# Kernel tuning notes

Hardware: AMD Instinct MI355X
Metric: run time of the kernel (lower is better)

Reference implementation:

```python
import jax, jax.numpy as jnp
import numpy as np

B, S, T, D_IN, D_T = 32, 4096, 8192, 128, 256


def _length_mask(key, batch, maxlen, minlen):
    lens = jax.random.randint(key, (batch,), minlen, maxlen + 1)
    lens = lens.at[0].set(maxlen)  # ensure max(t_lens)==maxlen (static t_len)
    return (jnp.arange(maxlen)[None, :] < lens[:, None]).astype(jnp.float32)


def setup_inputs() -> dict:
    key = jax.random.key(0)
    ks = jax.random.split(key, 8)
    student_emb = jax.random.normal(ks[0], (B, S, D_IN), dtype=jnp.float32)
    s_mask = _length_mask(ks[1], B, S, S // 2)
    t_mask = _length_mask(ks[2], B, T, T // 2)
    # params (stored as [in, out] so y = x @ W + b)
    pe_w1 = jax.random.normal(ks[3], (1, 64), dtype=jnp.float32) * 0.1
    pe_b1 = jnp.zeros((64,), dtype=jnp.float32)
    pe_w2 = jax.random.normal(ks[4], (64, D_IN), dtype=jnp.float32) * 0.1
    pe_b2 = jnp.zeros((D_IN,), dtype=jnp.float32)
    pt_w = jax.random.normal(ks[5], (2 * D_IN, D_T), dtype=jnp.float32) * 0.05
    pt_b = jnp.zeros((D_T,), dtype=jnp.float32)
    ln_g = jnp.ones((D_T,), dtype=jnp.float32)
    ln_b = jnp.zeros((D_T,), dtype=jnp.float32)
    neighbor_weights = jnp.ones((3,), dtype=jnp.float32)
    return {
        "student_emb": student_emb, "s_mask": s_mask, "t_mask": t_mask,
        "target_length": T,
        "pe_w1": pe_w1, "pe_b1": pe_b1, "pe_w2": pe_w2, "pe_b2": pe_b2,
        "pt_w": pt_w, "pt_b": pt_b, "ln_g": ln_g, "ln_b": ln_b,
        "neighbor_weights": neighbor_weights,
    }


def _layernorm(x, g, b, eps=1e-5):
    mu = jnp.mean(x, axis=-1, keepdims=True)
    var = jnp.mean(jnp.square(x - mu), axis=-1, keepdims=True)
    return (x - mu) * jax.lax.rsqrt(var + eps) * g + b


def reference(student_emb, s_mask, t_mask, target_length,
              pe_w1, pe_b1, pe_w2, pe_b2, pt_w, pt_b, ln_g, ln_b,
              neighbor_weights):
    batch, s_len, _ = student_emb.shape
    t_len = t_mask.shape[1]  # == max(t_mask.sum(1)) by construction
    s_lens = s_mask.sum(axis=1)  # [B] float
    pos = jnp.linspace(0.0, 1.0, t_len)  # [T]
    pos_grid = jnp.broadcast_to(pos[None, :], (batch, t_len))
    s_pos = pos_grid * (s_lens[:, None] - 1.0)
    curr = s_pos.astype(jnp.int32)                      # floor (nonneg)
    prev = jnp.clip(curr - 1, 0, s_len - 1)
    nxt = jnp.clip(curr + 1, 0, s_len - 1)

    def gat(idx):  # masked gather: [B,T,D]
        e = jnp.take_along_axis(student_emb, idx[..., None], axis=1)
        m = jnp.take_along_axis(s_mask, idx, axis=1)[..., None]
        return e * m

    w = jax.nn.softmax(neighbor_weights)
    blended = w[0] * gat(prev) + w[1] * gat(curr) + w[2] * gat(nxt)

    # position encoder MLP on scalar positions
    h = jax.nn.gelu(pos_grid[..., None] * pe_w1[0] + pe_b1, approximate=False)
    pos_emb = h @ pe_w2 + pe_b2  # [B,T,D_in]

    combined = jnp.concatenate([blended, pos_emb], axis=-1)  # [B,T,2*D_in]
    trans = jax.nn.gelu(combined @ pt_w + pt_b, approximate=False)
    trans = _layernorm(trans, ln_g, ln_b)
    trans = trans * t_mask[:, :t_len, None]
    if t_len < target_length:
        trans = jnp.pad(trans, ((0, 0), (0, target_length - t_len), (0, 0)))
    return trans
```

## Files before the change

### kernel.cpp

```cpp
#include <hip/hip_runtime.h>
#include <math.h>

#define S_LEN 4096
#define T_LEN 8192
#define D_TT  256
#define TILE_M 64
#define NKT   6
#define LDA   264

typedef unsigned short u16;
typedef __attribute__((ext_vector_type(8))) unsigned short u16x8;
typedef __attribute__((ext_vector_type(4))) float f32x4;
typedef __bf16 bf16x8 __attribute__((ext_vector_type(8)));

__device__ __forceinline__ float bf2f(u16 v) {
    union { unsigned u; float f; } x; x.u = ((unsigned)v) << 16; return x.f;
}
__device__ __forceinline__ u16 f2bf(float f) {
    union { float f; unsigned u; } x; x.f = f;
    return (u16)((x.u + 0x7fffu + ((x.u >> 16) & 1u)) >> 16);
}
__device__ __forceinline__ float gelu_f(float x) {
    return 0.5f * x * (1.0f + erff(x * 0.70710678118654752440f));
}

__device__ __forceinline__ bool detect_f32(const void* t_mask) {
    return *(const unsigned*)t_mask == 0x3F800000u;
}

template<bool F32>
__device__ __forceinline__ float ld1(const void* p, size_t i) {
    if constexpr (F32) return ((const float*)p)[i];
    else return bf2f(((const u16*)p)[i]);
}
template<bool F32>
__device__ __forceinline__ void load8(const void* p, size_t idx, float o[8]) {
    if constexpr (F32) {
        const float4* q = (const float4*)((const float*)p + idx);
        float4 a = q[0], b = q[1];
        o[0]=a.x; o[1]=a.y; o[2]=a.z; o[3]=a.w;
        o[4]=b.x; o[5]=b.y; o[6]=b.z; o[7]=b.w;
    } else {
        u16x8 v = *(const u16x8*)((const u16*)p + idx);
        #pragma unroll
        for (int j = 0; j < 8; ++j) o[j] = bf2f(v[j]);
    }
}
template<bool F32>
__device__ __forceinline__ void store8(void* p, size_t idx, const float o[8]) {
    if constexpr (F32) {
        float4 a = {o[0],o[1],o[2],o[3]};
        float4 b = {o[4],o[5],o[6],o[7]};
        float4* q = (float4*)((float*)p + idx);
        q[0] = a; q[1] = b;
    } else {
        u16x8 v;
        #pragma unroll
        for (int j = 0; j < 8; ++j) v[j] = f2bf(o[j]);
        *(u16x8*)((u16*)p + idx) = v;
    }
}


template<bool F32>
__global__ __launch_bounds__(256) void prep_kernel(
    const void* __restrict__ s_mask, const void* __restrict__ t_mask_det,
    const void* __restrict__ nw,
    const void* __restrict__ pe_w2, const void* __restrict__ pe_b2,
    const void* __restrict__ pt_w, const void* __restrict__ pt_b,
    int* __restrict__ ws_len, float* __restrict__ ws_w,
    float* __restrict__ ws_bias, u16* __restrict__ ws_bfrag)
{
    if (detect_f32(t_mask_det) != F32) return;
    int bi = blockIdx.x;
    int tid = threadIdx.x;
    if (bi < 32) {
        __shared__ float red[256];
        float s = 0.f;
        for (int i = tid; i < S_LEN; i += 256) s += ld1<F32>(s_mask, (size_t)bi * S_LEN + i);
        red[tid] = s;
        __syncthreads();
        for (int off = 128; off > 0; off >>= 1) {
            if (tid < off) red[tid] += red[tid + off];
            __syncthreads();
        }
        if (tid == 0) ws_len[bi] = (int)(red[0] + 0.5f);
    } else if (bi == 32) {
        if (tid == 0) {
            float a = ld1<F32>(nw, 0), b = ld1<F32>(nw, 1), c = ld1<F32>(nw, 2);
            float m = fmaxf(a, fmaxf(b, c));
            float ea = expf(a - m), eb = expf(b - m), ec = expf(c - m);
            float inv = 1.0f / (ea + eb + ec);
            ws_w[0] = ea * inv; ws_w[1] = eb * inv; ws_w[2] = ec * inv;
        }
    } else if (bi == 33) {
        int n = tid;
        float acc = ld1<F32>(pt_b, n);
        for (int d = 0; d < 128; ++d)
            acc += ld1<F32>(pe_b2, d) * ld1<F32>(pt_w, (size_t)(128 + d) * D_TT + n);
        ws_bias[n] = acc;
    } else if (bi < 42) {
        int t0 = (bi - 34) * 256 + tid;
        #pragma unroll
        for (int i = 0; i < 8; ++i) {
            int e = t0 + i * 2048;
            int j = e >> 8;
            int n = e & 255;
            float acc = 0.f;
            for (int d = 0; d < 128; ++d)
                acc += ld1<F32>(pe_w2, (size_t)j * 128 + d)
                     * ld1<F32>(pt_w, (size_t)(128 + d) * D_TT + n);
            int kt = 4 + (j >> 5);
            int q  = (j >> 3) & 3;
            int jj = j & 7;
            int nt = n >> 4;
            int lm = n & 15;
            int f = kt * 16 + nt;
            int lane = q * 16 + lm;
            ws_bfrag[((size_t)f * 64 + lane) * 8 + jj] = f2bf(acc);
        }
    } else {
        int g = (bi - 42) * 256 + tid;
        int f = g >> 6;
        int lane = g & 63;
        int kt = f >> 4, nt = f & 15;
        int q = lane >> 4, lm = lane & 15;
        u16x8 v;
        #pragma unroll
        for (int jj = 0; jj < 8; ++jj) {
            int k = kt * 32 + q * 8 + jj;
            int n = nt * 16 + lm;
            v[jj] = f2bf(ld1<F32>(pt_w, (size_t)k * D_TT + n));
        }
        *(u16x8*)(ws_bfrag + ((size_t)f * 64 + lane) * 8) = v;
    }
}

template<bool F32>
__global__ __launch_bounds__(256) void main_kernel(
    const void* __restrict__ emb, const void* __restrict__ s_mask,
    const void* __restrict__ t_mask,
    const void* __restrict__ pe_w1, const void* __restrict__ pe_b1,
    const void* __restrict__ ln_g, const void* __restrict__ ln_b,
    const int* __restrict__ ws_len, const float* __restrict__ ws_w,
    const float* __restrict__ ws_bias, const u16* __restrict__ ws_bfrag,
    void* __restrict__ out)
{
    if (detect_f32(t_mask) != F32) return;

    __shared__ __align__(16) u16 ldsC[TILE_M * LDA];
    __shared__ float ldsPartS[64][4];
    __shared__ float ldsPartQ[64][4];
    __shared__ float ldsMu[64];
    __shared__ float ldsRstd[64];

    int tid = threadIdx.x;
    int b = blockIdx.x >> 7;
    int tile = blockIdx.x & 127;
    int t0 = tile * TILE_M;

    int Li = ws_len[b];
    float w0 = ws_w[0], w1 = ws_w[1], w2 = ws_w[2];

    {
        int tt = tid >> 2, sub = tid & 3;
        int t = t0 + tt;
        const float step = 1.0f / 8191.0f;
        float posf = (float)t * step;
        float sp = posf * (float)(Li - 1);
        int ci = (int)sp;
        if (ci > S_LEN - 1) ci = S_LEN - 1;
        int pi = ci - 1; if (pi < 0) pi = 0;
        int ni = ci + 1; if (ni > S_LEN - 1) ni = S_LEN - 1;
        float mp = ld1<F32>(s_mask, (size_t)b * S_LEN + pi);
        float mc = ld1<F32>(s_mask, (size_t)b * S_LEN + ci);
        float mn = ld1<F32>(s_mask, (size_t)b * S_LEN + ni);
        float wp = w0 * mp, wc = w1 * mc, wn = w2 * mn;
        size_t Ep = ((size_t)b * S_LEN + pi) * 128;
        size_t Ec = ((size_t)b * S_LEN + ci) * 128;
        size_t En = ((size_t)b * S_LEN + ni) * 128;
        #pragma unroll
        for (int c = 0; c < 4; ++c) {
            int col = c * 32 + sub * 8;
            float vp[8], vc[8], vn[8];
            load8<F32>(emb, Ep + col, vp);
            load8<F32>(emb, Ec + col, vc);
            load8<F32>(emb, En + col, vn);
            u16x8 o;
            #pragma unroll
            for (int j = 0; j < 8; ++j)
                o[j] = f2bf(wp * vp[j] + wc * vc[j] + wn * vn[j]);
            *(u16x8*)(&ldsC[tt * LDA + col]) = o;
        }
        #pragma unroll
        for (int half = 0; half < 2; ++half) {
            u16x8 hv;
            #pragma unroll
            for (int jj = 0; jj < 8; ++jj) {
                int j = sub * 16 + half * 8 + jj;
                float x = posf * ld1<F32>(pe_w1, j) + ld1<F32>(pe_b1, j);
                hv[jj] = f2bf(gelu_f(x));
            }
            *(u16x8*)(&ldsC[tt * LDA + 128 + sub * 16 + half * 8]) = hv;
        }
    }
    __syncthreads();

    int lane = tid & 63, wv = tid >> 6;
    int q = lane >> 4, lm = lane & 15;
    f32x4 acc[4][4];
    #pragma unroll
    for (int m = 0; m < 4; ++m)
        #pragma unroll
        for (int n = 0; n < 4; ++n) acc[m][n] = (f32x4){0.f, 0.f, 0.f, 0.f};

    #pragma unroll
    for (int kt = 0; kt < NKT; ++kt) {
        bf16x8 a[4];
        #pragma unroll
        for (int m = 0; m < 4; ++m)
            a[m] = *(const bf16x8*)(&ldsC[(m * 16 + lm) * LDA + kt * 32 + q * 8]);
        #pragma unroll
        for (int n = 0; n < 4; ++n) {
            int nt = wv * 4 + n;
            bf16x8 bf = *(const bf16x8*)(ws_bfrag + ((size_t)(kt * 16 + nt) * 64 + lane) * 8);
            #pragma unroll
            for (int m = 0; m < 4; ++m)
                acc[m][n] = __builtin_amdgcn_mfma_f32_16x16x32_bf16(a[m], bf, acc[m][n], 0, 0, 0);
        }
    }
    __syncthreads();

    float bias[4];
    #pragma unroll
    for (int n = 0; n < 4; ++n) bias[n] = ws_bias[wv * 64 + n * 16 + lm];
    #pragma unroll
    for (int m = 0; m < 4; ++m)
        #pragma unroll
        for (int n = 0; n < 4; ++n)
            #pragma unroll
            for (int r = 0; r < 4; ++r) {
                float g = gelu_f(acc[m][n][r] + bias[n]);
                ldsC[(m * 16 + q * 4 + r) * LDA + wv * 64 + n * 16 + lm] = f2bf(g);
            }
    __syncthreads();

    {
        int tt = tid >> 2, part = tid & 3;
        float s = 0.f, sq = 0.f;
        #pragma unroll
        for (int c = 0; c < 8; ++c) {
            u16x8 v = *(u16x8*)(&ldsC[tt * LDA + part * 64 + c * 8]);
            #pragma unroll
            for (int j = 0; j < 8; ++j) { float g = bf2f(v[j]); s += g; sq += g * g; }
        }
        ldsPartS[tt][part] = s;
        ldsPartQ[tt][part] = sq;
    }
    __syncthreads();
    if (tid < 64) {
        float s  = ldsPartS[tid][0] + ldsPartS[tid][1] + ldsPartS[tid][2] + ldsPartS[tid][3];
        float sq = ldsPartQ[tid][0] + ldsPartQ[tid][1] + ldsPartQ[tid][2] + ldsPartQ[tid][3];
        float mu = s * (1.0f / 256.0f);
        float var = sq * (1.0f / 256.0f) - mu * mu;
        ldsMu[tid] = mu;
        ldsRstd[tid] = rsqrtf(var + 1e-5f);
    }
    __syncthreads();

    {
        int tt = tid >> 2, part = tid & 3;
        float mu = ldsMu[tt], rs = ldsRstd[tt];
        float tm = ld1<F32>(t_mask, (size_t)b * T_LEN + t0 + tt);
        size_t rowbase = (((size_t)b * T_LEN) + t0 + tt) * D_TT;
        #pragma unroll
        for (int c = 0; c < 8; ++c) {
            int col = c * 32 + part * 8;
            u16x8 v = *(u16x8*)(&ldsC[tt * LDA + col]);
            float gv[8], bv[8], o[8];
            load8<F32>(ln_g, col, gv);
            load8<F32>(ln_b, col, bv);
            #pragma unroll
            for (int j = 0; j < 8; ++j) {
                float y = (bf2f(v[j]) - mu) * rs * gv[j] + bv[j];
                o[j] = y * tm;
            }
            store8<F32>(out, rowbase + col, o);
        }
    }
}

extern "C" void kernel_launch(void* const* d_in, const int* in_sizes, int n_in,
                              void* d_out, int out_size, void* d_ws, size_t ws_size,
                              hipStream_t stream)
{
    (void)in_sizes; (void)n_in; (void)out_size; (void)ws_size;
    const void* emb    = d_in[0];
    const void* s_mask = d_in[1];
    const void* t_mask = d_in[2];
    const void* pe_w1  = d_in[4];
    const void* pe_b1  = d_in[5];
    const void* pe_w2  = d_in[6];
    const void* pe_b2  = d_in[7];
    const void* pt_w   = d_in[8];
    const void* pt_b   = d_in[9];
    const void* ln_g   = d_in[10];
    const void* ln_b   = d_in[11];
    const void* nw     = d_in[12];

    char* ws = (char*)d_ws;
    int*   ws_len  = (int*)ws;
    float* ws_w    = (float*)(ws + 128);
    float* ws_bias = (float*)(ws + 256);
    u16*   ws_bfrag= (u16*)(ws + 1280);

    prep_kernel<false><<<58, 256, 0, stream>>>(s_mask, t_mask, nw, pe_w2, pe_b2,
                                               pt_w, pt_b, ws_len, ws_w, ws_bias, ws_bfrag);
    prep_kernel<true><<<58, 256, 0, stream>>>(s_mask, t_mask, nw, pe_w2, pe_b2,
                                              pt_w, pt_b, ws_len, ws_w, ws_bias, ws_bfrag);
    main_kernel<false><<<32 * (T_LEN / TILE_M), 256, 0, stream>>>(
        emb, s_mask, t_mask, pe_w1, pe_b1, ln_g, ln_b,
        ws_len, ws_w, ws_bias, ws_bfrag, d_out);
    main_kernel<true><<<32 * (T_LEN / TILE_M), 256, 0, stream>>>(
        emb, s_mask, t_mask, pe_w1, pe_b1, ln_g, ln_b,
        ws_len, ws_w, ws_bias, ws_bfrag, d_out);
}
```

Before: 472.4 us.

## Precompute batch-independent position contribution and shrink main GEMM to blended half

```diff
diff --git a/kernel.cpp b/kernel.cpp
--- a/kernel.cpp
+++ b/kernel.cpp
@@ -7,6 +7,8 @@
 #define TILE_M 64
 #define NKT   6
 #define LDA   264
+#define NKT4  4
+#define LDA_A 136
 
 typedef unsigned short u16;
 typedef __attribute__((ext_vector_type(8))) unsigned short u16x8;
@@ -23,6 +25,19 @@
 __device__ __forceinline__ float gelu_f(float x) {
     return 0.5f * x * (1.0f + erff(x * 0.70710678118654752440f));
 }
+__device__ __forceinline__ float gelu_fast(float x) {
+    float z = fabsf(x) * 0.70710678118654752440f;
+    float t = __builtin_amdgcn_rcpf(fmaf(0.3275911f, z, 1.0f));
+    float p = fmaf(t, 1.061405429f, -1.453152027f);
+    p = fmaf(t, p, 1.421413741f);
+    p = fmaf(t, p, -0.284496736f);
+    p = fmaf(t, p, 0.254829592f);
+    p = p * t;
+    float e = __expf(-z * z);
+    float er = fmaf(-p, e, 1.0f);
+    er = copysignf(er, x);
+    return 0.5f * x * (1.0f + er);
+}
 
 __device__ __forceinline__ bool detect_f32(const void* t_mask) {
     return *(const unsigned*)t_mask == 0x3F800000u;
@@ -32,6 +47,11 @@
 __device__ __forceinline__ float ld1(const void* p, size_t i) {
     if constexpr (F32) return ((const float*)p)[i];
     else return bf2f(((const u16*)p)[i]);
+}
+template<bool F32>
+__device__ __forceinline__ void st1(void* p, size_t i, float v) {
+    if constexpr (F32) ((float*)p)[i] = v;
+    else ((u16*)p)[i] = f2bf(v);
 }
 template<bool F32>
 __device__ __forceinline__ void load8(const void* p, size_t idx, float o[8]) {
@@ -63,7 +83,267 @@
 
 
 template<bool F32>
-__global__ __launch_bounds__(256) void prep_kernel(
+__global__ __launch_bounds__(256) void prep_a(
+    const void* __restrict__ s_mask, const void* __restrict__ t_mask_det,
+    const void* __restrict__ nw,
+    const void* __restrict__ pe_w2, const void* __restrict__ pe_b2,
+    const void* __restrict__ pt_w, const void* __restrict__ pt_b,
+    int* __restrict__ ws_len, float* __restrict__ ws_w,
+    float* __restrict__ ws_bias, float* __restrict__ ws_w2p,
+    u16* __restrict__ ws_bfrag)
+{
+    if (detect_f32(t_mask_det) != F32) return;
+    int bi = blockIdx.x;
+    int tid = threadIdx.x;
+    if (bi < 32) {
+        __shared__ float red[256];
+        float s = 0.f;
+        for (int i = tid; i < S_LEN; i += 256) s += ld1<F32>(s_mask, (size_t)bi * S_LEN + i);
+        red[tid] = s;
+        __syncthreads();
+        for (int off = 128; off > 0; off >>= 1) {
+            if (tid < off) red[tid] += red[tid + off];
+            __syncthreads();
+        }
+        if (tid == 0) ws_len[bi] = (int)(red[0] + 0.5f);
+    } else if (bi == 32) {
+        if (tid == 0) {
+            float a = ld1<F32>(nw, 0), b = ld1<F32>(nw, 1), c = ld1<F32>(nw, 2);
+            float m = fmaxf(a, fmaxf(b, c));
+            float ea = expf(a - m), eb = expf(b - m), ec = expf(c - m);
+            float inv = 1.0f / (ea + eb + ec);
+            ws_w[0] = ea * inv; ws_w[1] = eb * inv; ws_w[2] = ec * inv;
+        }
+    } else if (bi < 41) {
+        __shared__ float pw[8 * 128];
+        int j0 = (bi - 33) * 8;
+        for (int i = tid; i < 1024; i += 256) pw[i] = ld1<F32>(pe_w2, (size_t)j0 * 128 + i);
+        __syncthreads();
+        int n = tid;
+        float acc[8];
+        #pragma unroll
+        for (int i = 0; i < 8; ++i) acc[i] = 0.f;
+        for (int d = 0; d < 128; ++d) {
+            float w = ld1<F32>(pt_w, (size_t)(128 + d) * D_TT + n);
+            #pragma unroll
+            for (int i = 0; i < 8; ++i) acc[i] += pw[i * 128 + d] * w;
+        }
+        #pragma unroll
+        for (int i = 0; i < 8; ++i) ws_w2p[(size_t)(j0 + i) * D_TT + n] = acc[i];
+    } else if (bi == 41) {
+        __shared__ float pb[128];
+        for (int i = tid; i < 128; i += 256) pb[i] = ld1<F32>(pe_b2, i);
+        __syncthreads();
+        int n = tid;
+        float acc = ld1<F32>(pt_b, n);
+        for (int d = 0; d < 128; ++d)
+            acc += pb[d] * ld1<F32>(pt_w, (size_t)(128 + d) * D_TT + n);
+        ws_bias[n] = acc;
+    } else {
+        int g = (bi - 42) * 256 + tid;
+        int f = g >> 6;
+        int lane = g & 63;
+        int kt = f >> 4, nt = f & 15;
+        int q = lane >> 4, lm = lane & 15;
+        u16x8 v;
+        #pragma unroll
+        for (int jj = 0; jj < 8; ++jj) {
+            int k = kt * 32 + q * 8 + jj;
+            int n = nt * 16 + lm;
+            v[jj] = f2bf(ld1<F32>(pt_w, (size_t)k * D_TT + n));
+        }
+        *(u16x8*)(ws_bfrag + ((size_t)f * 64 + lane) * 8) = v;
+    }
+}
+
+template<bool F32>
+__global__ __launch_bounds__(256) void prep_b(
+    const void* __restrict__ t_mask_det,
+    const void* __restrict__ pe_w1, const void* __restrict__ pe_b1,
+    const float* __restrict__ ws_bias, const float* __restrict__ ws_w2p,
+    float* __restrict__ posc)
+{
+    if (detect_f32(t_mask_det) != F32) return;
+    __shared__ float w2[64 * 256];
+    __shared__ float hl[16 * 64];
+    int tid = threadIdx.x;
+    int T0 = blockIdx.x * 16;
+    for (int i = tid; i < 4096; i += 256)
+        ((float4*)w2)[i] = ((const float4*)ws_w2p)[i];
+    for (int k = tid; k < 1024; k += 256) {
+        int tl = k >> 6, j = k & 63;
+        float posf = (float)(T0 + tl) * (1.0f / 8191.0f);
+        float x = posf * ld1<F32>(pe_w1, j) + ld1<F32>(pe_b1, j);
+        hl[k] = gelu_f(x);
+    }
+    __syncthreads();
+    int n = tid;
+    float bias = ws_bias[n];
+    float acc[16];
+    #pragma unroll
+    for (int tl = 0; tl < 16; ++tl) acc[tl] = bias;
+    for (int j = 0; j < 64; ++j) {
+        float w = w2[j * 256 + n];
+        #pragma unroll
+        for (int tl = 0; tl < 16; ++tl) acc[tl] += hl[tl * 64 + j] * w;
+    }
+    #pragma unroll
+    for (int tl = 0; tl < 16; ++tl)
+        posc[(size_t)(T0 + tl) * D_TT + n] = acc[tl];
+}
+
+template<bool F32>
+__global__ __launch_bounds__(256, 5) void main_fast(
+    const void* __restrict__ emb, const void* __restrict__ s_mask,
+    const void* __restrict__ t_mask,
+    const void* __restrict__ ln_g, const void* __restrict__ ln_b,
+    const int* __restrict__ ws_len, const float* __restrict__ ws_w,
+    const u16* __restrict__ ws_bfrag, const float* __restrict__ posc,
+    void* __restrict__ out)
+{
+    if (detect_f32(t_mask) != F32) return;
+
+    __shared__ __align__(16) u16 ldsA[TILE_M * LDA_A];
+    __shared__ float ldsPartS[TILE_M][4];
+    __shared__ float ldsPartQ[TILE_M][4];
+    __shared__ float ldsMu[TILE_M];
+    __shared__ float ldsRstd[TILE_M];
+    __shared__ float ldsTm[TILE_M];
+
+    int tid = threadIdx.x;
+    int b = blockIdx.x >> 7;
+    int tile = blockIdx.x & 127;
+    int t0 = tile * TILE_M;
+
+    int Li = ws_len[b];
+    float w0 = ws_w[0], w1 = ws_w[1], w2_ = ws_w[2];
+
+    {
+        int tt = tid >> 2, sub = tid & 3;
+        int t = t0 + tt;
+        const float step = 1.0f / 8191.0f;
+        float posf = (float)t * step;
+        float sp = posf * (float)(Li - 1);
+        int ci = (int)sp;
+        if (ci > S_LEN - 1) ci = S_LEN - 1;
+        int pi = ci - 1; if (pi < 0) pi = 0;
+        int ni = ci + 1; if (ni > S_LEN - 1) ni = S_LEN - 1;
+        float mp = ld1<F32>(s_mask, (size_t)b * S_LEN + pi);
+        float mc = ld1<F32>(s_mask, (size_t)b * S_LEN + ci);
+        float mn = ld1<F32>(s_mask, (size_t)b * S_LEN + ni);
+        float wp = w0 * mp, wc = w1 * mc, wn = w2_ * mn;
+        size_t Ep = ((size_t)b * S_LEN + pi) * 128;
+        size_t Ec = ((size_t)b * S_LEN + ci) * 128;
+        size_t En = ((size_t)b * S_LEN + ni) * 128;
+        #pragma unroll
+        for (int c = 0; c < 4; ++c) {
+            int col = c * 32 + sub * 8;
+            float vp[8], vc[8], vn[8];
+            load8<F32>(emb, Ep + col, vp);
+            load8<F32>(emb, Ec + col, vc);
+            load8<F32>(emb, En + col, vn);
+            u16x8 o;
+            #pragma unroll
+            for (int j = 0; j < 8; ++j)
+                o[j] = f2bf(wp * vp[j] + wc * vc[j] + wn * vn[j]);
+            *(u16x8*)(&ldsA[tt * LDA_A + col]) = o;
+        }
+        if (sub == 0) ldsTm[tt] = ld1<F32>(t_mask, (size_t)b * T_LEN + t);
+    }
+    __syncthreads();
+
+    int lane = tid & 63, wv = tid >> 6;
+    int q = lane >> 4, lm = lane & 15;
+    f32x4 acc[4][4];
+    #pragma unroll
+    for (int m = 0; m < 4; ++m)
+        #pragma unroll
+        for (int n = 0; n < 4; ++n) acc[m][n] = (f32x4){0.f, 0.f, 0.f, 0.f};
+
+    #pragma unroll
+    for (int kt = 0; kt < NKT4; ++kt) {
+        bf16x8 a[4];
+        #pragma unroll
+        for (int m = 0; m < 4; ++m)
+            a[m] = *(const bf16x8*)(&ldsA[(m * 16 + lm) * LDA_A + kt * 32 + q * 8]);
+        #pragma unroll
+        for (int n = 0; n < 4; ++n) {
+            int nt = wv * 4 + n;
+            bf16x8 bf = *(const bf16x8*)(ws_bfrag + ((size_t)(kt * 16 + nt) * 64 + lane) * 8);
+            #pragma unroll
+            for (int m = 0; m < 4; ++m)
+                acc[m][n] = __builtin_amdgcn_mfma_f32_16x16x32_bf16(a[m], bf, acc[m][n], 0, 0, 0);
+        }
+    }
+
+    int baseCol = wv * 64 + lm;
+    float gcol[4], bcol[4];
+    #pragma unroll
+    for (int n = 0; n < 4; ++n) {
+        gcol[n] = ld1<F32>(ln_g, baseCol + n * 16);
+        bcol[n] = ld1<F32>(ln_b, baseCol + n * 16);
+    }
+
+    #pragma unroll
+    for (int m = 0; m < 4; ++m) {
+        int r0 = m * 16 + q * 4;
+        const float* pc = posc + ((size_t)(t0 + r0)) * D_TT + baseCol;
+        float ps[4], pq[4];
+        #pragma unroll
+        for (int r = 0; r < 4; ++r) { ps[r] = 0.f; pq[r] = 0.f; }
+        #pragma unroll
+        for (int n = 0; n < 4; ++n)
+            #pragma unroll
+            for (int r = 0; r < 4; ++r) {
+                float v = acc[m][n][r] + pc[(size_t)r * D_TT + n * 16];
+                float g = gelu_fast(v);
+                acc[m][n][r] = g;
+                ps[r] += g;
+                pq[r] += g * g;
+            }
+        #pragma unroll
+        for (int off = 1; off < 16; off <<= 1)
+            #pragma unroll
+            for (int r = 0; r < 4; ++r) {
+                ps[r] += __shfl_xor(ps[r], off, 16);
+                pq[r] += __shfl_xor(pq[r], off, 16);
+            }
+        if (lm == 0) {
+            #pragma unroll
+            for (int r = 0; r < 4; ++r) {
+                ldsPartS[r0 + r][wv] = ps[r];
+                ldsPartQ[r0 + r][wv] = pq[r];
+            }
+        }
+    }
+    __syncthreads();
+    if (tid < 64) {
+        float s  = ldsPartS[tid][0] + ldsPartS[tid][1] + ldsPartS[tid][2] + ldsPartS[tid][3];
+        float sq = ldsPartQ[tid][0] + ldsPartQ[tid][1] + ldsPartQ[tid][2] + ldsPartQ[tid][3];
+        float mu = s * (1.0f / 256.0f);
+        float var = sq * (1.0f / 256.0f) - mu * mu;
+        ldsMu[tid] = mu;
+        ldsRstd[tid] = rsqrtf(var + 1e-5f);
+    }
+    __syncthreads();
+
+    size_t outRow0 = ((size_t)b * T_LEN + t0) * D_TT;
+    #pragma unroll
+    for (int m = 0; m < 4; ++m)
+        #pragma unroll
+        for (int r = 0; r < 4; ++r) {
+            int row = m * 16 + q * 4 + r;
+            float mu = ldsMu[row], rs = ldsRstd[row], tm = ldsTm[row];
+            #pragma unroll
+            for (int n = 0; n < 4; ++n) {
+                float y = (acc[m][n][r] - mu) * rs * gcol[n] + bcol[n];
+                st1<F32>(out, outRow0 + (size_t)row * D_TT + baseCol + n * 16, y * tm);
+            }
+        }
+}
+
+template<bool F32>
+__global__ __launch_bounds__(256) void legacy_prep_kernel(
     const void* __restrict__ s_mask, const void* __restrict__ t_mask_det,
     const void* __restrict__ nw,
     const void* __restrict__ pe_w2, const void* __restrict__ pe_b2,
@@ -111,12 +391,12 @@
                 acc += ld1<F32>(pe_w2, (size_t)j * 128 + d)
                      * ld1<F32>(pt_w, (size_t)(128 + d) * D_TT + n);
             int kt = 4 + (j >> 5);
-            int q  = (j >> 3) & 3;
+            int qq = (j >> 3) & 3;
             int jj = j & 7;
             int nt = n >> 4;
-            int lm = n & 15;
+            int lmm = n & 15;
             int f = kt * 16 + nt;
-            int lane = q * 16 + lm;
+            int lane = qq * 16 + lmm;
             ws_bfrag[((size_t)f * 64 + lane) * 8 + jj] = f2bf(acc);
         }
     } else {
@@ -124,12 +404,12 @@
         int f = g >> 6;
         int lane = g & 63;
         int kt = f >> 4, nt = f & 15;
-        int q = lane >> 4, lm = lane & 15;
+        int qq = lane >> 4, lmm = lane & 15;
         u16x8 v;
         #pragma unroll
         for (int jj = 0; jj < 8; ++jj) {
-            int k = kt * 32 + q * 8 + jj;
-            int n = nt * 16 + lm;
+            int k = kt * 32 + qq * 8 + jj;
+            int n = nt * 16 + lmm;
             v[jj] = f2bf(ld1<F32>(pt_w, (size_t)k * D_TT + n));
         }
         *(u16x8*)(ws_bfrag + ((size_t)f * 64 + lane) * 8) = v;
@@ -137,7 +417,7 @@
 }
 
 template<bool F32>
-__global__ __launch_bounds__(256) void main_kernel(
+__global__ __launch_bounds__(256) void legacy_main_kernel(
     const void* __restrict__ emb, const void* __restrict__ s_mask,
     const void* __restrict__ t_mask,
     const void* __restrict__ pe_w1, const void* __restrict__ pe_b1,
@@ -294,7 +574,7 @@
                               void* d_out, int out_size, void* d_ws, size_t ws_size,
                               hipStream_t stream)
 {
-    (void)in_sizes; (void)n_in; (void)out_size; (void)ws_size;
+    (void)in_sizes; (void)n_in; (void)out_size;
     const void* emb    = d_in[0];
     const void* s_mask = d_in[1];
     const void* t_mask = d_in[2];
@@ -309,19 +589,46 @@
     const void* nw     = d_in[12];
 
     char* ws = (char*)d_ws;
-    int*   ws_len  = (int*)ws;
-    float* ws_w    = (float*)(ws + 128);
-    float* ws_bias = (float*)(ws + 256);
-    u16*   ws_bfrag= (u16*)(ws + 1280);
-
-    prep_kernel<false><<<58, 256, 0, stream>>>(s_mask, t_mask, nw, pe_w2, pe_b2,
-                                               pt_w, pt_b, ws_len, ws_w, ws_bias, ws_bfrag);
-    prep_kernel<true><<<58, 256, 0, stream>>>(s_mask, t_mask, nw, pe_w2, pe_b2,
-                                              pt_w, pt_b, ws_len, ws_w, ws_bias, ws_bfrag);
-    main_kernel<false><<<32 * (T_LEN / TILE_M), 256, 0, stream>>>(
-        emb, s_mask, t_mask, pe_w1, pe_b1, ln_g, ln_b,
-        ws_len, ws_w, ws_bias, ws_bfrag, d_out);
-    main_kernel<true><<<32 * (T_LEN / TILE_M), 256, 0, stream>>>(
-        emb, s_mask, t_mask, pe_w1, pe_b1, ln_g, ln_b,
-        ws_len, ws_w, ws_bias, ws_bfrag, d_out);
-}
+    const size_t OFF_LEN   = 0;
+    const size_t OFF_W     = 128;
+    const size_t OFF_BIAS  = 256;
+    const size_t OFF_BFRAG = 1280;
+    const size_t OFF_W2P   = 66816;
+    const size_t OFF_POSC  = 132352;
+    const size_t WS_NEED   = OFF_POSC + (size_t)T_LEN * D_TT * 4;
+
+    if (ws_size >= WS_NEED) {
+        int*   ws_len   = (int*)(ws + OFF_LEN);
+        float* ws_w     = (float*)(ws + OFF_W);
+        float* ws_bias  = (float*)(ws + OFF_BIAS);
+        u16*   ws_bfrag = (u16*)(ws + OFF_BFRAG);
+        float* ws_w2p   = (float*)(ws + OFF_W2P);
+        float* posc     = (float*)(ws + OFF_POSC);
+
+        prep_a<false><<<58, 256, 0, stream>>>(s_mask, t_mask, nw, pe_w2, pe_b2,
+                                              pt_w, pt_b, ws_len, ws_w, ws_bias, ws_w2p, ws_bfrag);
+        prep_a<true><<<58, 256, 0, stream>>>(s_mask, t_mask, nw, pe_w2, pe_b2,
+                                             pt_w, pt_b, ws_len, ws_w, ws_bias, ws_w2p, ws_bfrag);
+        prep_b<false><<<T_LEN / 16, 256, 0, stream>>>(t_mask, pe_w1, pe_b1, ws_bias, ws_w2p, posc);
+        prep_b<true><<<T_LEN / 16, 256, 0, stream>>>(t_mask, pe_w1, pe_b1, ws_bias, ws_w2p, posc);
+        main_fast<false><<<32 * (T_LEN / TILE_M), 256, 0, stream>>>(
+            emb, s_mask, t_mask, ln_g, ln_b, ws_len, ws_w, ws_bfrag, posc, d_out);
+        main_fast<true><<<32 * (T_LEN / TILE_M), 256, 0, stream>>>(
+            emb, s_mask, t_mask, ln_g, ln_b, ws_len, ws_w, ws_bfrag, posc, d_out);
+    } else {
+        int*   ws_len   = (int*)ws;
+        float* ws_w     = (float*)(ws + 128);
+        float* ws_bias  = (float*)(ws + 256);
+        u16*   ws_bfrag = (u16*)(ws + 1280);
+        legacy_prep_kernel<false><<<58, 256, 0, stream>>>(s_mask, t_mask, nw, pe_w2, pe_b2,
+                                                          pt_w, pt_b, ws_len, ws_w, ws_bias, ws_bfrag);
+        legacy_prep_kernel<true><<<58, 256, 0, stream>>>(s_mask, t_mask, nw, pe_w2, pe_b2,
+                                                         pt_w, pt_b, ws_len, ws_w, ws_bias, ws_bfrag);
+        legacy_main_kernel<false><<<32 * (T_LEN / TILE_M), 256, 0, stream>>>(
+            emb, s_mask, t_mask, pe_w1, pe_b1, ln_g, ln_b,
+            ws_len, ws_w, ws_bias, ws_bfrag, d_out);
+        legacy_main_kernel<true><<<32 * (T_LEN / TILE_M), 256, 0, stream>>>(
+            emb, s_mask, t_mask, pe_w1, pe_b1, ln_g, ln_b,
+            ws_len, ws_w, ws_bias, ws_bfrag, d_out);
+    }
+}
```

Result: slower. 507.8 us (+7.5%).
